# Optimization experiments

Hardware: AMD Instinct MI355X
Metric: run time of the kernel (lower is better)

Reference implementation:

```python
import jax, jax.numpy as jnp
import numpy as np

INPUT_DIM = 3072
D_MODEL = 128      # mamba_hidden_dim
EXPAND = 2
D_INNER = EXPAND * D_MODEL   # 256
D_STATE = 16
D_CONV = 4
DT_RANK = D_MODEL // 16      # 8
NUM_LANES = 6
B, L = 4, 2048


def rmsnorm(x, w, eps=1e-5):
    return x * jax.lax.rsqrt(jnp.mean(x * x, axis=-1, keepdims=True) + eps) * w


def mamba_block(x, W_in, conv_w, conv_b, W_x, W_dt, b_dt, A_log, Dp, W_out):
    # x: [B, L, D_MODEL]
    bsz, seqlen, _ = x.shape
    xz = x @ W_in                              # [B, L, 2*D_INNER]
    xs, res = jnp.split(xz, 2, axis=-1)        # each [B, L, D_INNER]

    # depthwise causal conv1d over time
    xc = jnp.transpose(xs, (0, 2, 1))          # [B, C, L]
    k = conv_w[:, None, :]                     # [C, 1, K]
    xc = jax.lax.conv_general_dilated(
        xc, k, window_strides=(1,), padding=[(D_CONV - 1, 0)],
        dimension_numbers=('NCH', 'OIH', 'NCH'), feature_group_count=D_INNER)
    xc = xc + conv_b[None, :, None]
    xs = jax.nn.silu(jnp.transpose(xc, (0, 2, 1)))  # [B, L, C]

    # input-dependent SSM parameters
    dbl = xs @ W_x                             # [B, L, DT_RANK + 2*D_STATE]
    dt = dbl[..., :DT_RANK]
    Bm = dbl[..., DT_RANK:DT_RANK + D_STATE]   # [B, L, S]
    Cm = dbl[..., DT_RANK + D_STATE:]          # [B, L, S]
    delta = jax.nn.softplus(dt @ W_dt + b_dt)  # [B, L, C]

    A = -jnp.exp(A_log)                        # [C, S]
    dA = jnp.exp(delta[..., None] * A)                           # [B, L, C, S]
    dBu = delta[..., None] * Bm[:, :, None, :] * xs[..., None]   # [B, L, C, S]

    def step(h, inp):
        dA_t, dBu_t, C_t = inp                 # [B,C,S], [B,C,S], [B,S]
        h = dA_t * h + dBu_t
        y = jnp.einsum('bcs,bs->bc', h, C_t)
        return h, y

    h0 = jnp.zeros((bsz, D_INNER, D_STATE), x.dtype)
    _, ys = jax.lax.scan(
        step, h0,
        (jnp.moveaxis(dA, 1, 0), jnp.moveaxis(dBu, 1, 0), jnp.moveaxis(Cm, 1, 0)))
    y = jnp.moveaxis(ys, 0, 1) + xs * Dp       # [B, L, C]
    y = y * jax.nn.silu(res)
    return y @ W_out                           # [B, L, D_MODEL]


def setup_inputs() -> dict:
    key = jax.random.key(0)
    ks = jax.random.split(key, 12)
    s = 0.02
    inp = {
        'x': jax.random.normal(ks[0], (B, L, INPUT_DIM), jnp.float32),
        'W_emb': jax.random.normal(ks[1], (INPUT_DIM, D_MODEL), jnp.float32) * s,
        'b_emb': jnp.zeros((D_MODEL,), jnp.float32),
        'norm_w': jnp.ones((D_MODEL,), jnp.float32),
        'W_in': jax.random.normal(ks[2], (D_MODEL, 2 * D_INNER), jnp.float32) * s,
        'conv_w': jax.random.normal(ks[3], (D_INNER, D_CONV), jnp.float32) * 0.1,
        'conv_b': jnp.zeros((D_INNER,), jnp.float32),
        'W_x': jax.random.normal(ks[4], (D_INNER, DT_RANK + 2 * D_STATE), jnp.float32) * s,
        'W_dt': jax.random.normal(ks[5], (DT_RANK, D_INNER), jnp.float32) * s,
        'b_dt': jnp.full((D_INNER,), -2.0, jnp.float32),
        'A_log': jnp.log(jnp.broadcast_to(jnp.arange(1, D_STATE + 1, dtype=jnp.float32), (D_INNER, D_STATE))),
        'Dp': jnp.ones((D_INNER,), jnp.float32),
        'W_out': jax.random.normal(ks[6], (D_INNER, D_MODEL), jnp.float32) * s,
        'normf_w': jnp.ones((D_MODEL,), jnp.float32),
        'W_head': jax.random.normal(ks[7], (D_MODEL, NUM_LANES), jnp.float32) * s,
        'b_head': jnp.zeros((NUM_LANES,), jnp.float32),
    }
    return inp


def reference(x, W_emb, b_emb, norm_w, W_in, conv_w, conv_b, W_x, W_dt, b_dt,
              A_log, Dp, W_out, normf_w, W_head, b_head):
    h = x @ W_emb + b_emb                        # project 3072 -> 128
    h = h + mamba_block(rmsnorm(h, norm_w), W_in, conv_w, conv_b, W_x, W_dt,
                        b_dt, A_log, Dp, W_out)  # residual Mamba block
    Fm = rmsnorm(h, normf_w)
    # dropout is identity in eval
    out = Fm @ W_head + b_head                   # [B, L, NUM_LANES]
    pi = jax.nn.softmax(out, axis=-1)
    lane_preds = jnp.argmax(pi, axis=-1)
    return pi, lane_preds
```

## Files before the change

kernel.cpp:

```cpp
#include <hip/hip_runtime.h>
#include <hip/hip_bf16.h>
#include <math.h>

constexpr int B_ = 4, L_ = 2048, IN_DIM = 3072, DM = 128, DI = 256, DS = 16, NL = 6;
constexpr int ROWS = B_ * L_;
constexpr int SPLITK = 12, KC = IN_DIM / SPLITK;

static __device__ __forceinline__ float silu_f(float x) {
  return x / (1.f + __expf(-x));
}

__global__ __launch_bounds__(256) void gemm_emb_splitk(const float* __restrict__ A,
                                                       const float* __restrict__ Bv,
                                                       float* __restrict__ part) {
  constexpr int BM = 64, BK = 32;
  __shared__ float As[BK][BM + 4];
  __shared__ float Bs[BK][128 + 4];
  int split = blockIdx.x;
  int bm = blockIdx.y * BM;
  int kb = split * KC;
  int tid = threadIdx.x;
  int tm = tid >> 4, tn = tid & 15;

  float4 pa[2], pb[4];
#define EMB_PRELOAD(K0)                                                                  \
  {                                                                                      \
    _Pragma("unroll") for (int p = 0; p < 2; ++p) {                                      \
      int i = tid + p * 256;                                                             \
      int r = i >> 3, kq = (i & 7) * 4;                                                  \
      pa[p] = *(const float4*)&A[(size_t)(bm + r) * IN_DIM + kb + (K0) + kq];            \
    }                                                                                    \
    _Pragma("unroll") for (int p = 0; p < 4; ++p) {                                      \
      int i = tid + p * 256;                                                             \
      int r = i >> 5, c = (i & 31) * 4;                                                  \
      pb[p] = *(const float4*)&Bv[(size_t)(kb + (K0) + r) * DM + c];                     \
    }                                                                                    \
  }

  float acc[4][8] = {};
  EMB_PRELOAD(0);
  for (int k0 = 0; k0 < KC; k0 += BK) {
    __syncthreads();
#pragma unroll
    for (int p = 0; p < 2; ++p) {
      int i = tid + p * 256;
      int r = i >> 3, kq = (i & 7) * 4;
      As[kq + 0][r] = pa[p].x;
      As[kq + 1][r] = pa[p].y;
      As[kq + 2][r] = pa[p].z;
      As[kq + 3][r] = pa[p].w;
    }
#pragma unroll
    for (int p = 0; p < 4; ++p) {
      int i = tid + p * 256;
      int r = i >> 5, c = (i & 31) * 4;
      *(float4*)&Bs[r][c] = pb[p];
    }
    __syncthreads();
    if (k0 + BK < KC) EMB_PRELOAD(k0 + BK);
#pragma unroll
    for (int kk = 0; kk < BK; ++kk) {
      float4 a4 = *(const float4*)&As[kk][tm * 4];
      float4 b0 = *(const float4*)&Bs[kk][tn * 4];
      float4 b1 = *(const float4*)&Bs[kk][64 + tn * 4];
      float a[4] = {a4.x, a4.y, a4.z, a4.w};
      float b[8] = {b0.x, b0.y, b0.z, b0.w, b1.x, b1.y, b1.z, b1.w};
#pragma unroll
      for (int i = 0; i < 4; ++i)
#pragma unroll
        for (int j = 0; j < 8; ++j) acc[i][j] = fmaf(a[i], b[j], acc[i][j]);
    }
  }
#undef EMB_PRELOAD
#pragma unroll
  for (int i = 0; i < 4; ++i) {
    size_t rowoff = ((size_t)split * ROWS + bm + tm * 4 + i) * DM;
    float4 o0 = {acc[i][0], acc[i][1], acc[i][2], acc[i][3]};
    float4 o1 = {acc[i][4], acc[i][5], acc[i][6], acc[i][7]};
    *(float4*)&part[rowoff + tn * 4] = o0;
    *(float4*)&part[rowoff + 64 + tn * 4] = o1;
  }
}

__global__ __launch_bounds__(256) void reduce_rms_kernel(const float* __restrict__ part,
                                                         const float* __restrict__ b_emb,
                                                         const float* __restrict__ norm_w,
                                                         float* __restrict__ h0,
                                                         float* __restrict__ u) {
  int wave = threadIdx.x >> 6, lane = threadIdx.x & 63;
  int row = blockIdx.x * 4 + wave;
  float sx = 0.f, sy = 0.f;
#pragma unroll
  for (int sp = 0; sp < SPLITK; ++sp) {
    float2 v = *(const float2*)(part + ((size_t)sp * ROWS + row) * DM + 2 * lane);
    sx += v.x;
    sy += v.y;
  }
  float2 be = *(const float2*)(b_emb + 2 * lane);
  sx += be.x;
  sy += be.y;
  float2 hv = {sx, sy};
  *(float2*)(h0 + (size_t)row * DM + 2 * lane) = hv;
  float ss = sx * sx + sy * sy;
#pragma unroll
  for (int o = 32; o >= 1; o >>= 1) ss += __shfl_xor(ss, o);
  float rs = 1.f / sqrtf(ss * (1.f / 128.f) + 1e-5f);
  float2 wv = *(const float2*)(norm_w + 2 * lane);
  float2 o2 = {sx * rs * wv.x, sy * rs * wv.y};
  *(float2*)(u + (size_t)row * DM + 2 * lane) = o2;
}

__global__ __launch_bounds__(256) void gemm_in(const float* __restrict__ A,
                                               const float* __restrict__ Bv,
                                               float* __restrict__ C) {
  constexpr int BK = 32, N = 512;
  __shared__ float As[BK][32 + 4];
  __shared__ float Bs[BK][128 + 4];
  int bn = blockIdx.x * 128;
  int bm = blockIdx.y * 32;
  int tid = threadIdx.x;
  int tm = tid >> 4, tn = tid & 15;

  float4 pa, pb[4];
#define IN_PRELOAD(K0)                                                                   \
  {                                                                                      \
    int r = tid >> 3, kq = (tid & 7) * 4;                                                \
    pa = *(const float4*)&A[(size_t)(bm + r) * DM + (K0) + kq];                          \
    _Pragma("unroll") for (int p = 0; p < 4; ++p) {                                      \
      int i = tid + p * 256;                                                             \
      int rr = i >> 5, c = (i & 31) * 4;                                                 \
      pb[p] = *(const float4*)&Bv[(size_t)((K0) + rr) * N + bn + c];                     \
    }                                                                                    \
  }

  float acc[2][8] = {};
  IN_PRELOAD(0);
  for (int k0 = 0; k0 < DM; k0 += BK) {
    __syncthreads();
    {
      int r = tid >> 3, kq = (tid & 7) * 4;
      As[kq + 0][r] = pa.x;
      As[kq + 1][r] = pa.y;
      As[kq + 2][r] = pa.z;
      As[kq + 3][r] = pa.w;
    }
#pragma unroll
    for (int p = 0; p < 4; ++p) {
      int i = tid + p * 256;
      int rr = i >> 5, c = (i & 31) * 4;
      *(float4*)&Bs[rr][c] = pb[p];
    }
    __syncthreads();
    if (k0 + BK < DM) IN_PRELOAD(k0 + BK);
#pragma unroll
    for (int kk = 0; kk < BK; ++kk) {
      float2 a2 = *(const float2*)&As[kk][tm * 2];
      float4 b0 = *(const float4*)&Bs[kk][tn * 4];
      float4 b1 = *(const float4*)&Bs[kk][64 + tn * 4];
      float b[8] = {b0.x, b0.y, b0.z, b0.w, b1.x, b1.y, b1.z, b1.w};
#pragma unroll
      for (int j = 0; j < 8; ++j) acc[0][j] = fmaf(a2.x, b[j], acc[0][j]);
#pragma unroll
      for (int j = 0; j < 8; ++j) acc[1][j] = fmaf(a2.y, b[j], acc[1][j]);
    }
  }
#undef IN_PRELOAD
#pragma unroll
  for (int i = 0; i < 2; ++i) {
    size_t rowoff = (size_t)(bm + tm * 2 + i) * N + bn;
    float4 o0 = {acc[i][0], acc[i][1], acc[i][2], acc[i][3]};
    float4 o1 = {acc[i][4], acc[i][5], acc[i][6], acc[i][7]};
    *(float4*)&C[rowoff + tn * 4] = o0;
    *(float4*)&C[rowoff + 64 + tn * 4] = o1;
  }
}

__global__ __launch_bounds__(256) void conv_silu_kernel(const float* __restrict__ xz,
                                                        const float* __restrict__ conv_w,
                                                        const float* __restrict__ conv_b,
                                                        float* __restrict__ xs_row,
                                                        float* __restrict__ xs_T) {
  __shared__ float tile[64][65];
  __shared__ float cw[64][4];
  __shared__ float cb[64];
  int b = blockIdx.z, l0 = blockIdx.y * 64, c0 = blockIdx.x * 64;
  int tid = threadIdx.x;
  cw[tid / 4][tid % 4] = conv_w[(size_t)c0 * 4 + tid];
  if (tid < 64) cb[tid] = conv_b[c0 + tid];
  __syncthreads();
  int cl = tid % 64;
  int lbase = tid / 64;
#pragma unroll
  for (int i = 0; i < 16; ++i) {
    int ll = lbase + 4 * i;
    int l = l0 + ll;
    float acc = cb[cl];
#pragma unroll
    for (int k = 0; k < 4; ++k) {
      int li = l + k - 3;
      if (li >= 0) acc = fmaf(xz[((size_t)(b * L_ + li)) * 512 + c0 + cl], cw[cl][k], acc);
    }
    tile[ll][cl] = silu_f(acc);
  }
  __syncthreads();
  for (int i = tid; i < 4096; i += 256) {
    int lr = i / 64, c = i % 64;
    xs_row[((size_t)(b * L_ + l0 + lr)) * DI + c0 + c] = tile[lr][c];
  }
  for (int i = tid; i < 4096; i += 256) {
    int c = i / 64, lr = i % 64;
    xs_T[((size_t)(b * DI + c0 + c)) * L_ + l0 + lr] = tile[lr][c];
  }
}

__global__ __launch_bounds__(256) void dbl_kernel(const float* __restrict__ xs_row,
                                                  const float* __restrict__ W_x,
                                                  float* __restrict__ dbl) {
  __shared__ float Xs[32][257];
  __shared__ float Wx[256 * 40];
  int tid = threadIdx.x;
  int r0 = blockIdx.x * 32;
  for (int i = tid; i < 32 * 64; i += 256) {
    int r = i >> 6, kq = (i & 63) * 4;
    float4 v = *(const float4*)&xs_row[(size_t)(r0 + r) * DI + kq];
    Xs[r][kq + 0] = v.x;
    Xs[r][kq + 1] = v.y;
    Xs[r][kq + 2] = v.z;
    Xs[r][kq + 3] = v.w;
  }
  for (int i = tid; i < 256 * 40; i += 256) Wx[i] = W_x[i];
  __syncthreads();
  int r = tid & 31, q = tid >> 5;
  float acc[5] = {};
  for (int k = 0; k < 256; ++k) {
    float v = Xs[r][k];
#pragma unroll
    for (int j = 0; j < 5; ++j) acc[j] = fmaf(v, Wx[k * 40 + q * 5 + j], acc[j]);
  }
#pragma unroll
  for (int j = 0; j < 5; ++j) dbl[(size_t)(r0 + r) * 40 + q * 5 + j] = acc[j];
}

__global__ __launch_bounds__(256) void delta_kernel(const float* __restrict__ dbl,
                                                    const float* __restrict__ W_dt,
                                                    const float* __restrict__ b_dt,
                                                    float* __restrict__ delta_T) {
  __shared__ float Tile[32][257];
  __shared__ float Dt[32][8];
  __shared__ float Wdt[8 * 256];
  int tid = threadIdx.x;
  int r0 = blockIdx.x * 32;
  int b = r0 / L_, l0 = r0 % L_;
  if (tid < 256) {
    int r = tid >> 3, k = tid & 7;
    Dt[r][k] = dbl[(size_t)(r0 + r) * 40 + k];
  }
  for (int i = tid; i < 8 * 256; i += 256) Wdt[i] = W_dt[i];
  __syncthreads();
  int c = tid;
  float bd = b_dt[c];
  for (int r = 0; r < 32; ++r) {
    float a = bd;
#pragma unroll
    for (int k = 0; k < 8; ++k) a = fmaf(Dt[r][k], Wdt[k * 256 + c], a);
    float sp = (a > 20.f) ? a : log1pf(__expf(a));
    Tile[r][c] = sp;
  }
  __syncthreads();
  for (int i = tid; i < 32 * 256; i += 256) {
    int cc = i >> 5, rr = i & 31;
    delta_T[((size_t)(b * DI + cc)) * L_ + l0 + rr] = Tile[rr][cc];
  }
}

__global__ __launch_bounds__(512) void scan_kernel(const float* __restrict__ delta_T,
                                                   const float* __restrict__ xs_T,
                                                   const float* __restrict__ dbl,
                                                   const float* __restrict__ A_log,
                                                   const float* __restrict__ Dp,
                                                   const float* __restrict__ xz,
                                                   float* __restrict__ y) {
  __shared__ float s_aprod[32][16];
  __shared__ float s_hend[32][16];
  __shared__ float s_hstart[32][16];
  int tid = threadIdx.x;
  int k = tid >> 4, s = tid & 15;
  int g = blockIdx.x;
  int b = g >> 8, c = g & 255;
  float A = -__expf(A_log[c * DS + s]);
  float dpc = Dp[c];
  const float* dp = delta_T + (size_t)g * L_ + k * 64;
  const float* xp = xs_T + (size_t)g * L_ + k * 64;
  const float* bp = dbl + ((size_t)(b * L_ + k * 64)) * 40 + 8 + s;
  const float* cp = dbl + ((size_t)(b * L_ + k * 64)) * 40 + 24 + s;

  float aprod = 1.f, h = 0.f;
  for (int j = 0; j < 64; j += 4) {
    float4 d4 = *(const float4*)(dp + j);
    float4 x4 = *(const float4*)(xp + j);
    float dj[4] = {d4.x, d4.y, d4.z, d4.w};
    float xj[4] = {x4.x, x4.y, x4.z, x4.w};
#pragma unroll
    for (int u = 0; u < 4; ++u) {
      float Bv = bp[(size_t)(j + u) * 40];
      float dA = __expf(dj[u] * A);
      aprod *= dA;
      h = fmaf(dA, h, dj[u] * Bv * xj[u]);
    }
  }
  s_aprod[k][s] = aprod;
  s_hend[k][s] = h;
  __syncthreads();

  if (tid < 16) {
    float hh = 0.f;
    for (int kk = 0; kk < 32; ++kk) {
      s_hstart[kk][tid] = hh;
      hh = fmaf(s_aprod[kk][tid], hh, s_hend[kk][tid]);
    }
  }
  __syncthreads();

  h = s_hstart[k][s];
  float* yp = y + ((size_t)(b * L_) + k * 64) * DI + c;
  const float* rp = xz + ((size_t)(b * L_) + k * 64) * 512 + 256 + c;
  for (int j = 0; j < 64; j += 4) {
    float4 d4 = *(const float4*)(dp + j);
    float4 x4 = *(const float4*)(xp + j);
    float dj[4] = {d4.x, d4.y, d4.z, d4.w};
    float xj[4] = {x4.x, x4.y, x4.z, x4.w};
#pragma unroll
    for (int u = 0; u < 4; ++u) {
      float Bv = bp[(size_t)(j + u) * 40];
      float Cv = cp[(size_t)(j + u) * 40];
      float dA = __expf(dj[u] * A);
      h = fmaf(dA, h, dj[u] * Bv * xj[u]);
      float p = h * Cv;
      p += __shfl_xor(p, 8, 16);
      p += __shfl_xor(p, 4, 16);
      p += __shfl_xor(p, 2, 16);
      p += __shfl_xor(p, 1, 16);
      if (s == 0) {
        float res = rp[(size_t)(j + u) * 512];
        yp[(size_t)(j + u) * DI] = (p + xj[u] * dpc) * silu_f(res);
      }
    }
  }
}

__global__ __launch_bounds__(256) void final_gemm_kernel(const float* __restrict__ y,
                                                         const float* __restrict__ W_out,
                                                         const float* __restrict__ h0,
                                                         const float* __restrict__ normf_w,
                                                         const float* __restrict__ W_head,
                                                         const float* __restrict__ b_head,
                                                         float* __restrict__ pi_out,
                                                         float* __restrict__ pred_out) {
  constexpr int BK = 32;
  __shared__ float As[BK][16 + 4];
  __shared__ float Bs[BK][128 + 4];
  __shared__ float Wh[128 * 6];
  int tid = threadIdx.x;
  int tm = tid >> 4, tn = tid & 15;
  int bm = blockIdx.x * 16;
  for (int i = tid; i < 768; i += 256) Wh[i] = W_head[i];

  float4 pa, pb[4];
#define FN_PRELOAD(K0)                                                                   \
  {                                                                                      \
    if (tid < 128) {                                                                     \
      int r = tid >> 3, kq = (tid & 7) * 4;                                              \
      pa = *(const float4*)&y[(size_t)(bm + r) * DI + (K0) + kq];                        \
    }                                                                                    \
    _Pragma("unroll") for (int p = 0; p < 4; ++p) {                                      \
      int i = tid + p * 256;                                                             \
      int rr = i >> 5, c = (i & 31) * 4;                                                 \
      pb[p] = *(const float4*)&W_out[(size_t)((K0) + rr) * DM + c];                      \
    }                                                                                    \
  }

  float acc[8] = {};
  FN_PRELOAD(0);
  for (int k0 = 0; k0 < DI; k0 += BK) {
    __syncthreads();
    if (tid < 128) {
      int r = tid >> 3, kq = (tid & 7) * 4;
      As[kq + 0][r] = pa.x;
      As[kq + 1][r] = pa.y;
      As[kq + 2][r] = pa.z;
      As[kq + 3][r] = pa.w;
    }
#pragma unroll
    for (int p = 0; p < 4; ++p) {
      int i = tid + p * 256;
      int rr = i >> 5, c = (i & 31) * 4;
      *(float4*)&Bs[rr][c] = pb[p];
    }
    __syncthreads();
    if (k0 + BK < DI) FN_PRELOAD(k0 + BK);
#pragma unroll
    for (int kk = 0; kk < BK; ++kk) {
      float a0 = As[kk][tm];
      float4 b0 = *(const float4*)&Bs[kk][tn * 4];
      float4 b1 = *(const float4*)&Bs[kk][64 + tn * 4];
      float b[8] = {b0.x, b0.y, b0.z, b0.w, b1.x, b1.y, b1.z, b1.w};
#pragma unroll
      for (int j = 0; j < 8; ++j) acc[j] = fmaf(a0, b[j], acc[j]);
    }
  }
#undef FN_PRELOAD
  float4 nwa = *(const float4*)&normf_w[tn * 4];
  float4 nwb = *(const float4*)&normf_w[64 + tn * 4];
  float nw[8] = {nwa.x, nwa.y, nwa.z, nwa.w, nwb.x, nwb.y, nwb.z, nwb.w};
  float bh[6];
#pragma unroll
  for (int j = 0; j < 6; ++j) bh[j] = b_head[j];
  int row = bm + tm;
  float4 h0a = *(const float4*)&h0[(size_t)row * DM + tn * 4];
  float4 h0b = *(const float4*)&h0[(size_t)row * DM + 64 + tn * 4];
  float hv[8] = {acc[0] + h0a.x, acc[1] + h0a.y, acc[2] + h0a.z, acc[3] + h0a.w,
                 acc[4] + h0b.x, acc[5] + h0b.y, acc[6] + h0b.z, acc[7] + h0b.w};
  float ss = 0.f;
#pragma unroll
  for (int j = 0; j < 8; ++j) ss += hv[j] * hv[j];
  ss += __shfl_xor(ss, 1);
  ss += __shfl_xor(ss, 2);
  ss += __shfl_xor(ss, 4);
  ss += __shfl_xor(ss, 8);
  float rs = 1.f / sqrtf(ss * (1.f / 128.f) + 1e-5f);
  float lg[6] = {};
#pragma unroll
  for (int j = 0; j < 8; ++j) {
    float fm = hv[j] * rs * nw[j];
    int col = (j < 4) ? (tn * 4 + j) : (64 + tn * 4 + (j - 4));
#pragma unroll
    for (int l = 0; l < 6; ++l) lg[l] = fmaf(fm, Wh[col * 6 + l], lg[l]);
  }
#pragma unroll
  for (int l = 0; l < 6; ++l) {
    lg[l] += __shfl_xor(lg[l], 1);
    lg[l] += __shfl_xor(lg[l], 2);
    lg[l] += __shfl_xor(lg[l], 4);
    lg[l] += __shfl_xor(lg[l], 8);
    lg[l] += bh[l];
  }
  if (tn == 0) {
    float mv = lg[0];
    int am = 0;
#pragma unroll
    for (int l = 1; l < 6; ++l)
      if (lg[l] > mv) { mv = lg[l]; am = l; }
    float e[6], sum = 0.f;
#pragma unroll
    for (int l = 0; l < 6; ++l) { e[l] = __expf(lg[l] - mv); sum += e[l]; }
    float inv = 1.f / sum;
#pragma unroll
    for (int l = 0; l < 6; ++l) pi_out[(size_t)row * NL + l] = e[l] * inv;
    pred_out[row] = (float)am;
  }
}

extern "C" void kernel_launch(void* const* d_in, const int* in_sizes, int n_in,
                              void* d_out, int out_size, void* d_ws, size_t ws_size,
                              hipStream_t stream) {
  const float* x = (const float*)d_in[0];
  const float* W_emb = (const float*)d_in[1];
  const float* b_emb = (const float*)d_in[2];
  const float* norm_w = (const float*)d_in[3];
  const float* W_in = (const float*)d_in[4];
  const float* conv_w = (const float*)d_in[5];
  const float* conv_b = (const float*)d_in[6];
  const float* W_x = (const float*)d_in[7];
  const float* W_dt = (const float*)d_in[8];
  const float* b_dt = (const float*)d_in[9];
  const float* A_log = (const float*)d_in[10];
  const float* Dp = (const float*)d_in[11];
  const float* W_out = (const float*)d_in[12];
  const float* normf_w = (const float*)d_in[13];
  const float* W_head = (const float*)d_in[14];
  const float* b_head = (const float*)d_in[15];

  float* ws = (float*)d_ws;
  float* h0 = ws;
  float* u = h0 + 1048576;
  float* xz = u + 1048576;
  float* xs_row = xz + 4194304;
  float* xs_T = xs_row + 2097152;
  float* dbl = xs_T + 2097152;
  float* delta_T = dbl + 327680;
  float* y = delta_T + 2097152;

  float* part = xz;

  float* pi_out = (float*)d_out;
  float* pred_out = pi_out + (size_t)ROWS * NL;

  gemm_emb_splitk<<<dim3(SPLITK, ROWS / 64), 256, 0, stream>>>(x, W_emb, part);
  reduce_rms_kernel<<<ROWS / 4, 256, 0, stream>>>(part, b_emb, norm_w, h0, u);
  gemm_in<<<dim3(4, 256), 256, 0, stream>>>(u, W_in, xz);
  conv_silu_kernel<<<dim3(4, 32, 4), 256, 0, stream>>>(xz, conv_w, conv_b, xs_row, xs_T);
  dbl_kernel<<<256, 256, 0, stream>>>(xs_row, W_x, dbl);
  delta_kernel<<<256, 256, 0, stream>>>(dbl, W_dt, b_dt, delta_T);
  scan_kernel<<<1024, 512, 0, stream>>>(delta_T, xs_T, dbl, A_log, Dp, xz, y);
  final_gemm_kernel<<<512, 256, 0, stream>>>(y, W_out, h0, normf_w, W_head, b_head, pi_out, pred_out);
}
```

Measured before the change: 446.2 us.

## Drop emb GEMM prefetch, cut split-K, shrink dbl/delta tiles for more blocks

The embedding GEMM loses its register double-buffer prefetch, now loads global memory straight into shared memory with a sync on each side, and uses 8 split-K slices instead of 12. The dbl and delta kernels move from 32-row to 8-row tiles and launch 1024 blocks, so more workgroups run on the GPU. dbl_kernel stops staging W_x in shared memory and reads it from global (cached) memory, with one output column per thread. The intent is more occupancy and parallelism in the small kernels, at the cost of less latency hiding in the large GEMM and a delta_T store pattern with shorter contiguous runs.

New measurement: 493.4 us. 1.11x slower.

```diff
diff --git a/kernel.cpp b/kernel.cpp
--- a/kernel.cpp
+++ b/kernel.cpp
@@ -4,7 +4,7 @@
 
 constexpr int B_ = 4, L_ = 2048, IN_DIM = 3072, DM = 128, DI = 256, DS = 16, NL = 6;
 constexpr int ROWS = B_ * L_;
-constexpr int SPLITK = 12, KC = IN_DIM / SPLITK;
+constexpr int SPLITK = 8, KC = IN_DIM / SPLITK;
 
 static __device__ __forceinline__ float silu_f(float x) {
   return x / (1.f + __expf(-x));
@@ -21,43 +21,25 @@
   int kb = split * KC;
   int tid = threadIdx.x;
   int tm = tid >> 4, tn = tid & 15;
-
-  float4 pa[2], pb[4];
-#define EMB_PRELOAD(K0)                                                                  \
-  {                                                                                      \
-    _Pragma("unroll") for (int p = 0; p < 2; ++p) {                                      \
-      int i = tid + p * 256;                                                             \
-      int r = i >> 3, kq = (i & 7) * 4;                                                  \
-      pa[p] = *(const float4*)&A[(size_t)(bm + r) * IN_DIM + kb + (K0) + kq];            \
-    }                                                                                    \
-    _Pragma("unroll") for (int p = 0; p < 4; ++p) {                                      \
-      int i = tid + p * 256;                                                             \
-      int r = i >> 5, c = (i & 31) * 4;                                                  \
-      pb[p] = *(const float4*)&Bv[(size_t)(kb + (K0) + r) * DM + c];                     \
-    }                                                                                    \
-  }
-
   float acc[4][8] = {};
-  EMB_PRELOAD(0);
   for (int k0 = 0; k0 < KC; k0 += BK) {
-    __syncthreads();
 #pragma unroll
     for (int p = 0; p < 2; ++p) {
       int i = tid + p * 256;
       int r = i >> 3, kq = (i & 7) * 4;
-      As[kq + 0][r] = pa[p].x;
-      As[kq + 1][r] = pa[p].y;
-      As[kq + 2][r] = pa[p].z;
-      As[kq + 3][r] = pa[p].w;
+      float4 a4 = *(const float4*)&A[(size_t)(bm + r) * IN_DIM + kb + k0 + kq];
+      As[kq + 0][r] = a4.x;
+      As[kq + 1][r] = a4.y;
+      As[kq + 2][r] = a4.z;
+      As[kq + 3][r] = a4.w;
     }
 #pragma unroll
     for (int p = 0; p < 4; ++p) {
       int i = tid + p * 256;
       int r = i >> 5, c = (i & 31) * 4;
-      *(float4*)&Bs[r][c] = pb[p];
-    }
-    __syncthreads();
-    if (k0 + BK < KC) EMB_PRELOAD(k0 + BK);
+      *(float4*)&Bs[r][c] = *(const float4*)&Bv[(size_t)(kb + k0 + r) * DM + c];
+    }
+    __syncthreads();
 #pragma unroll
     for (int kk = 0; kk < BK; ++kk) {
       float4 a4 = *(const float4*)&As[kk][tm * 4];
@@ -70,8 +52,8 @@
 #pragma unroll
         for (int j = 0; j < 8; ++j) acc[i][j] = fmaf(a[i], b[j], acc[i][j]);
     }
-  }
-#undef EMB_PRELOAD
+    __syncthreads();
+  }
 #pragma unroll
   for (int i = 0; i < 4; ++i) {
     size_t rowoff = ((size_t)split * ROWS + bm + tm * 4 + i) * DM;
@@ -216,11 +198,10 @@
 __global__ __launch_bounds__(256) void dbl_kernel(const float* __restrict__ xs_row,
                                                   const float* __restrict__ W_x,
                                                   float* __restrict__ dbl) {
-  __shared__ float Xs[32][257];
-  __shared__ float Wx[256 * 40];
-  int tid = threadIdx.x;
-  int r0 = blockIdx.x * 32;
-  for (int i = tid; i < 32 * 64; i += 256) {
+  __shared__ float Xs[8][260];
+  int tid = threadIdx.x;
+  int r0 = blockIdx.x * 8;
+  for (int i = tid; i < 8 * 64; i += 256) {
     int r = i >> 6, kq = (i & 63) * 4;
     float4 v = *(const float4*)&xs_row[(size_t)(r0 + r) * DI + kq];
     Xs[r][kq + 0] = v.x;
@@ -228,30 +209,29 @@
     Xs[r][kq + 2] = v.z;
     Xs[r][kq + 3] = v.w;
   }
-  for (int i = tid; i < 256 * 40; i += 256) Wx[i] = W_x[i];
-  __syncthreads();
-  int r = tid & 31, q = tid >> 5;
-  float acc[5] = {};
+  __syncthreads();
+  int r = tid >> 5, q = tid & 31;
+  float acc0 = 0.f, acc1 = 0.f;
   for (int k = 0; k < 256; ++k) {
     float v = Xs[r][k];
-#pragma unroll
-    for (int j = 0; j < 5; ++j) acc[j] = fmaf(v, Wx[k * 40 + q * 5 + j], acc[j]);
-  }
-#pragma unroll
-  for (int j = 0; j < 5; ++j) dbl[(size_t)(r0 + r) * 40 + q * 5 + j] = acc[j];
+    acc0 = fmaf(v, W_x[k * 40 + q], acc0);
+    if (q < 8) acc1 = fmaf(v, W_x[k * 40 + 32 + q], acc1);
+  }
+  dbl[(size_t)(r0 + r) * 40 + q] = acc0;
+  if (q < 8) dbl[(size_t)(r0 + r) * 40 + 32 + q] = acc1;
 }
 
 __global__ __launch_bounds__(256) void delta_kernel(const float* __restrict__ dbl,
                                                     const float* __restrict__ W_dt,
                                                     const float* __restrict__ b_dt,
                                                     float* __restrict__ delta_T) {
-  __shared__ float Tile[32][257];
-  __shared__ float Dt[32][8];
+  __shared__ float Dt[8][8];
   __shared__ float Wdt[8 * 256];
-  int tid = threadIdx.x;
-  int r0 = blockIdx.x * 32;
+  __shared__ float Tile[8][257];
+  int tid = threadIdx.x;
+  int r0 = blockIdx.x * 8;
   int b = r0 / L_, l0 = r0 % L_;
-  if (tid < 256) {
+  if (tid < 64) {
     int r = tid >> 3, k = tid & 7;
     Dt[r][k] = dbl[(size_t)(r0 + r) * 40 + k];
   }
@@ -259,16 +239,16 @@
   __syncthreads();
   int c = tid;
   float bd = b_dt[c];
-  for (int r = 0; r < 32; ++r) {
+#pragma unroll
+  for (int r = 0; r < 8; ++r) {
     float a = bd;
 #pragma unroll
     for (int k = 0; k < 8; ++k) a = fmaf(Dt[r][k], Wdt[k * 256 + c], a);
-    float sp = (a > 20.f) ? a : log1pf(__expf(a));
-    Tile[r][c] = sp;
-  }
-  __syncthreads();
-  for (int i = tid; i < 32 * 256; i += 256) {
-    int cc = i >> 5, rr = i & 31;
+    Tile[r][c] = (a > 20.f) ? a : log1pf(__expf(a));
+  }
+  __syncthreads();
+  for (int i = tid; i < 8 * 256; i += 256) {
+    int cc = i >> 3, rr = i & 7;
     delta_T[((size_t)(b * DI + cc)) * L_ + l0 + rr] = Tile[rr][cc];
   }
 }
@@ -499,8 +479,8 @@
   reduce_rms_kernel<<<ROWS / 4, 256, 0, stream>>>(part, b_emb, norm_w, h0, u);
   gemm_in<<<dim3(4, 256), 256, 0, stream>>>(u, W_in, xz);
   conv_silu_kernel<<<dim3(4, 32, 4), 256, 0, stream>>>(xz, conv_w, conv_b, xs_row, xs_T);
-  dbl_kernel<<<256, 256, 0, stream>>>(xs_row, W_x, dbl);
-  delta_kernel<<<256, 256, 0, stream>>>(dbl, W_dt, b_dt, delta_T);
+  dbl_kernel<<<1024, 256, 0, stream>>>(xs_row, W_x, dbl);
+  delta_kernel<<<1024, 256, 0, stream>>>(dbl, W_dt, b_dt, delta_T);
   scan_kernel<<<1024, 512, 0, stream>>>(delta_T, xs_T, dbl, A_log, Dp, xz, y);
   final_gemm_kernel<<<512, 256, 0, stream>>>(y, W_out, h0, normf_w, W_head, b_head, pi_out, pred_out);
 }
```
